# Performance work log

Measured on AMD Instinct MI355X. Metric: run time of the kernel, lower is better.

The kernel has to match this reference:

```python
import jax, jax.numpy as jnp
import numpy as np

D = 768        # word_emb_dim * 3 (span embedding dim)
H = 1024       # assumed FFNNScore hidden width
K = 250        # antecedent window (self.k)
P_LAMBDA = 0.4


def setup_inputs() -> dict:
    key = jax.random.key(0)
    ks = jax.random.split(key, 8)
    N, T = 2000, 1000
    return {
        "vectors": jax.random.normal(ks[0], (N, D), jnp.float32),
        "Wm1": jax.random.normal(ks[1], (D, H), jnp.float32) / np.sqrt(D),
        "bm1": jnp.zeros((H,), jnp.float32),
        "wm2": jax.random.normal(ks[2], (H,), jnp.float32) / np.sqrt(H),
        "bm2": jnp.zeros((1,), jnp.float32),
        "Wp1": jax.random.normal(ks[3], (3 * D, H), jnp.float32) / np.sqrt(3 * D),
        "bp1": jnp.zeros((H,), jnp.float32),
        "wp2": jax.random.normal(ks[4], (H,), jnp.float32) / np.sqrt(H),
        "bp2": jnp.zeros((1,), jnp.float32),
        "span_starts": jax.random.randint(ks[5], (N,), 0, T, dtype=jnp.int32),
        "span_ends": jax.random.randint(ks[6], (N,), 0, T, dtype=jnp.int32),
        "t": T,
    }


def reference(vectors, Wm1, bm1, wm2, bm2, Wp1, bp1, wp2, bp2,
              span_starts, span_ends, t):
    m = int(P_LAMBDA * t)  # number of retained spans (static)

    # mention scorer: FFNN over all span embeddings  [N]
    scores = jax.nn.relu(vectors @ Wm1 + bm1) @ wm2 + bm2[0]

    # prune to top int(p_lambda * t) spans by mention score (descending sort)
    top = jnp.argsort(-scores)[:m]
    s_top, v_top = scores[top], vectors[top]

    # re-sort retained spans by (i_start, i_end) descending
    order = jnp.lexsort((span_ends[top], span_starts[top]))[::-1]
    v, s = v_top[order], s_top[order]  # [m, D], [m]

    # pairwise scorer weight split for cat([a, b, a*b]) @ Wp1
    Wa, Wb, Wab = Wp1[:D], Wp1[D:2 * D], Wp1[2 * D:]

    # antecedent windows: span i vs spans i+1 .. i+K (padded/masked)
    idx = jnp.arange(m - 1)[:, None] + 1 + jnp.arange(K)[None, :]  # [m-1, K]
    valid = idx < m
    idxc = jnp.minimum(idx, m - 1)

    a = v[:m - 1]                      # [m-1, D]
    b = v[idxc]                        # [m-1, K, D]
    hb = (v @ Wb)[idxc]                # gather precomputed b-projection [m-1, K, H]
    h = jax.nn.relu((a @ Wa)[:, None, :] + hb
                    + jnp.einsum('ikd,dh->ikh', a[:, None, :] * b, Wab)
                    + bp1)             # [m-1, K, H]
    pairwise = h @ wp2 + bp2[0]        # [m-1, K]

    ant = pairwise + s[idxc] + s[:m - 1, None]
    ant = jnp.where(valid, ant, -jnp.inf)
    # dummy antecedent (epsilon) score 0 appended, then softmax per span
    full = jnp.concatenate([ant, jnp.zeros((m - 1, 1), ant.dtype)], axis=1)
    return jax.nn.softmax(full, axis=-1)  # [m-1, K+1]
```

## Files before the change

kernel.cpp:

```cpp
#include <hip/hip_runtime.h>
#include <hip/hip_bf16.h>
#include <math.h>

#define NVEC 2000
#define DD   768
#define HH   1024
#define KNUM 250
#define MSEL 400
#define MR   399
#define OUTW 251
#define PPAD 256
#define NPAIR (MR * PPAD)
#define BM 128
#define BN 256
#define BK 64
#define NKT (DD / BK)
#define NNB (HH / BN)
#define KH1 271
#define PAIRBLKS (MR + KH1)

typedef short  bf16x8 __attribute__((ext_vector_type(8)));
typedef float  f32x4  __attribute__((ext_vector_type(4)));
typedef unsigned int u32;
typedef u32    u32x4  __attribute__((ext_vector_type(4)));

__device__ __forceinline__ float waveSum(float p) {
#pragma unroll
  for (int off = 32; off >= 1; off >>= 1) p += __shfl_xor(p, off, 64);
  return p;
}
__device__ __forceinline__ float waveMax(float p) {
#pragma unroll
  for (int off = 32; off >= 1; off >>= 1) p = fmaxf(p, __shfl_xor(p, off, 64));
  return p;
}
__device__ __forceinline__ short f2bf(float f) {
  __hip_bfloat16 h = __float2bfloat16(f);
  return __builtin_bit_cast(short, h);
}
__device__ __forceinline__ void gload_lds16(const void* g, void* l) {
  __builtin_amdgcn_global_load_lds(
      (const __attribute__((address_space(1))) u32*)g,
      (__attribute__((address_space(3))) u32*)l, 16, 0, 0);
}
__device__ __forceinline__ bf16x8 prodcvt(const float* av, bf16x8 b) {
  u32x4 u = __builtin_bit_cast(u32x4, b);
  bf16x8 r;
#pragma unroll
  for (int p = 0; p < 4; ++p) {
    const float blo = __builtin_bit_cast(float, u[p] << 16);
    const float bhi = __builtin_bit_cast(float, u[p] & 0xffff0000u);
    r[2 * p]     = f2bf(av[2 * p]     * blo);
    r[2 * p + 1] = f2bf(av[2 * p + 1] * bhi);
  }
  return r;
}

__global__ __launch_bounds__(512) void scores_kernel(
    const float* __restrict__ vectors, const float* __restrict__ Wm1,
    const float* __restrict__ bm1, const float* __restrict__ wm2,
    const float* __restrict__ bm2, float* __restrict__ scores) {
  __shared__ float vrow[8 * DD];
  __shared__ float red[8];
  const int tid = threadIdx.x;
  const int base = blockIdx.x * 8;
  for (int idx = tid; idx < 8 * DD; idx += 512)
    vrow[idx] = vectors[base * DD + idx];
  __syncthreads();
  float acc[8][2];
#pragma unroll
  for (int r = 0; r < 8; ++r) { acc[r][0] = 0.f; acc[r][1] = 0.f; }
#pragma unroll 4
  for (int d = 0; d < DD; ++d) {
    const float2 w = ((const float2*)(Wm1 + (size_t)d * HH))[tid];
#pragma unroll
    for (int r = 0; r < 8; ++r) {
      const float a = vrow[r * DD + d];
      acc[r][0] += a * w.x; acc[r][1] += a * w.y;
    }
  }
  const float2 b = ((const float2*)bm1)[tid];
  const float2 m = ((const float2*)wm2)[tid];
  const float sc = bm2[0];
  for (int r = 0; r < 8; ++r) {
    float p = fmaxf(acc[r][0] + b.x, 0.f) * m.x + fmaxf(acc[r][1] + b.y, 0.f) * m.y;
    p = waveSum(p);
    if ((tid & 63) == 0) red[tid >> 6] = p;
    __syncthreads();
    if (tid == 0) {
      float t = red[0];
#pragma unroll
      for (int w8 = 1; w8 < 8; ++w8) t += red[w8];
      scores[base + r] = t + sc;
    }
    __syncthreads();
  }
}

__global__ __launch_bounds__(1024) void sortwt_kernel(
    const float* __restrict__ scores, const int* __restrict__ sst,
    const int* __restrict__ sen, const float* __restrict__ Wp1,
    int* __restrict__ perm, float* __restrict__ sfin, ushort* __restrict__ Wt) {
  const int tid = threadIdx.x;
  if (blockIdx.x == 0) {
    __shared__ float ks[2048];
    __shared__ int   ki[2048];
    __shared__ int s_st[512], s_en[512], s_j[512];
    for (int e = tid; e < 2048; e += 1024) {
      ks[e] = (e < NVEC) ? scores[e] : -INFINITY;
      ki[e] = e;
    }
    __syncthreads();
    for (int k = 2; k <= 2048; k <<= 1) {
      for (int j = k >> 1; j > 0; j >>= 1) {
        for (int e = tid; e < 2048; e += 1024) {
          const int l = e ^ j;
          if (l > e) {
            const float s1 = ks[e], s2 = ks[l];
            const int i1 = ki[e], i2 = ki[l];
            const bool first = (s1 > s2) || (s1 == s2 && i1 < i2);
            const bool up = ((e & k) == 0);
            if (up ? !first : first) {
              ks[e] = s2; ks[l] = s1; ki[e] = i2; ki[l] = i1;
            }
          }
        }
        __syncthreads();
      }
    }
    for (int e = tid; e < 512; e += 1024) {
      if (e < MSEL) { const int ti = ki[e]; s_st[e] = sst[ti]; s_en[e] = sen[ti]; }
      else { s_st[e] = 0x7fffffff; s_en[e] = 0x7fffffff; }
      s_j[e] = e;
    }
    __syncthreads();
    for (int k = 2; k <= 512; k <<= 1) {
      for (int j = k >> 1; j > 0; j >>= 1) {
        for (int e = tid; e < 512; e += 1024) {
          const int l = e ^ j;
          if (l > e) {
            const int a0 = s_st[e], a1 = s_en[e], a2 = s_j[e];
            const int b0 = s_st[l], b1 = s_en[l], b2 = s_j[l];
            const bool first = (a0 < b0) || (a0 == b0 && (a1 < b1 || (a1 == b1 && a2 < b2)));
            const bool up = ((e & k) == 0);
            if (up ? !first : first) {
              s_st[e] = b0; s_en[e] = b1; s_j[e] = b2;
              s_st[l] = a0; s_en[l] = a1; s_j[l] = a2;
            }
          }
        }
        __syncthreads();
      }
    }
    for (int i = tid; i < MSEL; i += 1024) {
      const int src = s_j[MSEL - 1 - i];
      const int vi = ki[src];
      perm[i] = vi;
      sfin[i] = scores[vi];
    }
  } else {
    __shared__ float tile[64][65];
    const int t2 = blockIdx.x - 1;
    const int kb = t2 % 12;
    const int nb = t2 / 12;
    const float* Wab = Wp1 + 2 * DD * HH;
    for (int idx = tid; idx < 64 * 64; idx += 1024) {
      const int kk = idx >> 6, nn = idx & 63;
      tile[kk][nn] = Wab[(size_t)(kb * 64 + kk) * HH + nb * 64 + nn];
    }
    __syncthreads();
    for (int idx = tid; idx < 64 * 64; idx += 1024) {
      const int nn = idx >> 6, kk = idx & 63;
      Wt[(size_t)(nb * 64 + nn) * DD + kb * 64 + kk] = (ushort)f2bf(tile[kk][nn]);
    }
  }
}

__global__ __launch_bounds__(512) void hab_kernel(
    const float* __restrict__ vectors, const float* __restrict__ Wp1,
    const int* __restrict__ perm, float* __restrict__ Ha, float* __restrict__ Hv,
    float* __restrict__ Vp, ushort* __restrict__ Vpb) {
  __shared__ float vrow[8 * DD];
  const int tid = threadIdx.x;
  const int base = blockIdx.x * 8;
  const int mat = blockIdx.y >> 1;
  const int half = blockIdx.y & 1;
  for (int r = 0; r < 8; ++r) {
    const int pi = perm[base + r];
    for (int d = tid; d < DD; d += 512) {
      const float val = vectors[pi * DD + d];
      vrow[r * DD + d] = val;
      if (blockIdx.y == 0) {
        Vp[(size_t)(base + r) * DD + d] = val;
        Vpb[(size_t)(base + r) * DD + d] = (ushort)f2bf(val);
      }
    }
  }
  __syncthreads();
  float acc[8];
#pragma unroll
  for (int r = 0; r < 8; ++r) acc[r] = 0.f;
  const float* W = Wp1 + (size_t)mat * DD * HH + half * 512 + tid;
#pragma unroll 4
  for (int d = 0; d < DD; ++d) {
    const float w = W[(size_t)d * HH];
#pragma unroll
    for (int r = 0; r < 8; ++r) acc[r] += vrow[r * DD + d] * w;
  }
  float* dst = mat ? Hv : Ha;
  for (int r = 0; r < 8; ++r) {
    const int row = base + r;
    if (mat == 0 && row >= MR) continue;
    dst[(size_t)row * HH + half * 512 + tid] = acc[r];
  }
}

__global__ __launch_bounds__(512, 2) void pair_kernel(
    const float* __restrict__ Vp, const ushort* __restrict__ Vpb,
    const ushort* __restrict__ Wt,
    const float* __restrict__ bp1, const float* __restrict__ wp2,
    const float* __restrict__ Ha, const float* __restrict__ Hv,
    float* __restrict__ pp) {
  __shared__ __align__(16) ushort As[BM * BK];
  __shared__ __align__(16) ushort Bs[BN * BK];
  __shared__ float redp[BM][4];
  const int tid = threadIdx.x;
  const int bx = blockIdx.x;
  const int khalf = (bx < MR) ? 0 : 1;
  const int i = (bx < MR) ? bx : (bx - MR);
  const int nb = blockIdx.y;
  const int n0 = nb * BN;
  const int lane = tid & 63;
  const int wid = tid >> 6;
  const int wr = wid >> 2, wc = wid & 3;
  const int lhi = lane >> 4, llo = lane & 15;

  const int cs = tid & 7;
  const int rb9 = tid >> 3;
  const int csx = cs ^ (rb9 & 7);
  const ushort* vsrc[2];
  int rowA[2];
#pragma unroll
  for (int it = 0; it < 2; ++it) {
    rowA[it] = it * 64 + rb9;
    int j = i + 1 + khalf * BM + rowA[it];
    if (j > MR) j = MR;
    vsrc[it] = Vpb + (size_t)j * DD + cs * 8;
  }
  int rowB[4];
#pragma unroll
  for (int it = 0; it < 4; ++it) rowB[it] = it * 64 + rb9;
  const float* avp = Vp + (size_t)i * DD + cs * 8;

  f32x4 acc[4][4];
#pragma unroll
  for (int a = 0; a < 4; ++a)
#pragma unroll
    for (int b = 0; b < 4; ++b) acc[a][b] = (f32x4){0.f, 0.f, 0.f, 0.f};

  for (int kt = 0; kt < NKT; ++kt) {
    const int kg = kt * BK;
    bf16x8 bv[2];
    float av[8];
#pragma unroll
    for (int it = 0; it < 2; ++it) bv[it] = *(const bf16x8*)(vsrc[it] + kg);
    *(float4*)(av) = *(const float4*)(avp + kg);
    *(float4*)(av + 4) = *(const float4*)(avp + kg + 4);
#pragma unroll
    for (int it = 0; it < 4; ++it)
      gload_lds16(Wt + (size_t)(n0 + rowB[it]) * DD + kg + csx * 8,
                  (char*)Bs + (it * 512 + tid) * 16);
#pragma unroll
    for (int it = 0; it < 2; ++it)
      *(bf16x8*)((char*)As + rowA[it] * 128 + (csx << 4)) = prodcvt(av, bv[it]);
    __syncthreads();
#pragma unroll
    for (int ks = 0; ks < 2; ++ks) {
      bf16x8 af[4], bfr[4];
#pragma unroll
      for (int mi = 0; mi < 4; ++mi) {
        const int row = wr * 64 + mi * 16 + llo;
        const int ch = (ks * 4 + lhi) ^ (row & 7);
        af[mi] = *(const bf16x8*)((const char*)As + row * 128 + (ch << 4));
      }
#pragma unroll
      for (int ni = 0; ni < 4; ++ni) {
        const int row = wc * 64 + ni * 16 + llo;
        const int ch = (ks * 4 + lhi) ^ (row & 7);
        bfr[ni] = *(const bf16x8*)((const char*)Bs + row * 128 + (ch << 4));
      }
#pragma unroll
      for (int mi = 0; mi < 4; ++mi)
#pragma unroll
        for (int ni = 0; ni < 4; ++ni)
          acc[mi][ni] = __builtin_amdgcn_mfma_f32_16x16x32_bf16(af[mi], bfr[ni], acc[mi][ni], 0, 0, 0);
    }
    __syncthreads();
  }

  float hb4[4], wpv[4];
  int cg[4];
#pragma unroll
  for (int ni = 0; ni < 4; ++ni) {
    const int col = n0 + wc * 64 + ni * 16 + llo;
    cg[ni] = col;
    hb4[ni] = Ha[(size_t)i * HH + col] + bp1[col];
    wpv[ni] = wp2[col];
  }
#pragma unroll
  for (int mi = 0; mi < 4; ++mi) {
#pragma unroll
    for (int r = 0; r < 4; ++r) {
      const int rowl = wr * 64 + mi * 16 + lhi * 4 + r;
      int j = i + 1 + khalf * BM + rowl;
      if (j > MR) j = MR;
      float part = 0.f;
#pragma unroll
      for (int ni = 0; ni < 4; ++ni) {
        const float pre = acc[mi][ni][r] + hb4[ni] + Hv[(size_t)j * HH + cg[ni]];
        part += fmaxf(pre, 0.f) * wpv[ni];
      }
      part += __shfl_xor(part, 1, 64);
      part += __shfl_xor(part, 2, 64);
      part += __shfl_xor(part, 4, 64);
      part += __shfl_xor(part, 8, 64);
      if (llo == 0) redp[rowl][wc] = part;
    }
  }
  __syncthreads();
  if (tid < BM)
    pp[(size_t)nb * NPAIR + (size_t)i * PPAD + khalf * BM + tid] =
        redp[tid][0] + redp[tid][1] + redp[tid][2] + redp[tid][3];
}

__global__ __launch_bounds__(256) void softmax_kernel(
    const float* __restrict__ pp, const float* __restrict__ sfin,
    const float* __restrict__ bp2, float* __restrict__ out) {
  __shared__ float red[4];
  const int i = blockIdx.x, tid = threadIdx.x;
  float v;
  if (tid < KNUM) {
    const int jidx = i + 1 + tid;
    const bool valid = jidx < MSEL;
    const int jc = valid ? jidx : MR;
    float s = 0.f;
#pragma unroll
    for (int b = 0; b < NNB; ++b) s += pp[(size_t)b * NPAIR + i * PPAD + tid];
    v = valid ? (s + bp2[0] + sfin[jc] + sfin[i]) : -INFINITY;
  } else if (tid == KNUM) v = 0.f;
  else v = -INFINITY;
  float mx = waveMax(v);
  if ((tid & 63) == 0) red[tid >> 6] = mx;
  __syncthreads();
  const float m = fmaxf(fmaxf(red[0], red[1]), fmaxf(red[2], red[3]));
  __syncthreads();
  const float e = (tid <= KNUM) ? expf(v - m) : 0.f;
  float s = waveSum(e);
  if ((tid & 63) == 0) red[tid >> 6] = s;
  __syncthreads();
  const float tot = red[0] + red[1] + red[2] + red[3];
  if (tid <= KNUM) out[i * OUTW + tid] = e / tot;
}

extern "C" void kernel_launch(void* const* d_in, const int* in_sizes, int n_in,
                              void* d_out, int out_size, void* d_ws, size_t ws_size,
                              hipStream_t stream) {
  const float* vectors = (const float*)d_in[0];
  const float* Wm1 = (const float*)d_in[1];
  const float* bm1 = (const float*)d_in[2];
  const float* wm2 = (const float*)d_in[3];
  const float* bm2 = (const float*)d_in[4];
  const float* Wp1 = (const float*)d_in[5];
  const float* bp1 = (const float*)d_in[6];
  const float* wp2 = (const float*)d_in[7];
  const float* bp2 = (const float*)d_in[8];
  const int* sst = (const int*)d_in[9];
  const int* sen = (const int*)d_in[10];
  float* out = (float*)d_out;
  char* ws = (char*)d_ws;

  float* scores = (float*)(ws);
  int*   perm   = (int*)(ws + 10240);
  float* sfin   = (float*)(ws + 12288);
  float* Ha     = (float*)(ws + 16384);
  float* Hv     = (float*)(ws + 16384 + 1638400);
  float* Vp     = (float*)(ws + 3293184);
  ushort* Wt    = (ushort*)(ws + 4521984);
  ushort* Vpb   = (ushort*)(ws + 6094848);
  float* pp     = (float*)(ws + 6709248);

  scores_kernel<<<NVEC / 8, 512, 0, stream>>>(vectors, Wm1, bm1, wm2, bm2, scores);
  sortwt_kernel<<<193, 1024, 0, stream>>>(scores, sst, sen, Wp1, perm, sfin, Wt);
  hab_kernel<<<dim3(MSEL / 8, 4), 512, 0, stream>>>(vectors, Wp1, perm, Ha, Hv, Vp, Vpb);
  pair_kernel<<<dim3(PAIRBLKS, NNB), 512, 0, stream>>>(Vp, Vpb, Wt, bp1, wp2, Ha, Hv, pp);
  softmax_kernel<<<MR, 256, 0, stream>>>(pp, sfin, bp2, out);
}
```

Before: 357.0 us.

## Fuse softmax into pair kernel via last-block atomic counter; split scores over H

The softmax kernel is removed. Each pair block increments a per-row atomic counter after writing its partial, and the last block to arrive for a row does the reduction and softmax. This saves one launch and its tail. The scores kernel now splits the hidden dimension across two blocks with 16 rows each. The two partial sums are combined, with the bias added, in the sort kernel. This reshapes the scores grid and data reuse, at the cost of atomics, fences and an extra done-buffer reset in hab_kernel.

```diff
diff --git a/kernel.cpp b/kernel.cpp
--- a/kernel.cpp
+++ b/kernel.cpp
@@ -59,31 +59,29 @@
 __global__ __launch_bounds__(512) void scores_kernel(
     const float* __restrict__ vectors, const float* __restrict__ Wm1,
     const float* __restrict__ bm1, const float* __restrict__ wm2,
-    const float* __restrict__ bm2, float* __restrict__ scores) {
-  __shared__ float vrow[8 * DD];
+    float* __restrict__ spart) {
+  __shared__ float vrow[16 * DD];
   __shared__ float red[8];
   const int tid = threadIdx.x;
-  const int base = blockIdx.x * 8;
-  for (int idx = tid; idx < 8 * DD; idx += 512)
+  const int base = blockIdx.x * 16;
+  const int half = blockIdx.y;
+  for (int idx = tid; idx < 16 * DD; idx += 512)
     vrow[idx] = vectors[base * DD + idx];
   __syncthreads();
-  float acc[8][2];
-#pragma unroll
-  for (int r = 0; r < 8; ++r) { acc[r][0] = 0.f; acc[r][1] = 0.f; }
+  float acc[16];
+#pragma unroll
+  for (int r = 0; r < 16; ++r) acc[r] = 0.f;
+  const float* W = Wm1 + half * 512 + tid;
 #pragma unroll 4
   for (int d = 0; d < DD; ++d) {
-    const float2 w = ((const float2*)(Wm1 + (size_t)d * HH))[tid];
-#pragma unroll
-    for (int r = 0; r < 8; ++r) {
-      const float a = vrow[r * DD + d];
-      acc[r][0] += a * w.x; acc[r][1] += a * w.y;
-    }
-  }
-  const float2 b = ((const float2*)bm1)[tid];
-  const float2 m = ((const float2*)wm2)[tid];
-  const float sc = bm2[0];
-  for (int r = 0; r < 8; ++r) {
-    float p = fmaxf(acc[r][0] + b.x, 0.f) * m.x + fmaxf(acc[r][1] + b.y, 0.f) * m.y;
+    const float w = W[(size_t)d * HH];
+#pragma unroll
+    for (int r = 0; r < 16; ++r) acc[r] += vrow[r * DD + d] * w;
+  }
+  const float b = bm1[half * 512 + tid];
+  const float m = wm2[half * 512 + tid];
+  for (int r = 0; r < 16; ++r) {
+    float p = fmaxf(acc[r] + b, 0.f) * m;
     p = waveSum(p);
     if ((tid & 63) == 0) red[tid >> 6] = p;
     __syncthreads();
@@ -91,23 +89,26 @@
       float t = red[0];
 #pragma unroll
       for (int w8 = 1; w8 < 8; ++w8) t += red[w8];
-      scores[base + r] = t + sc;
+      spart[(size_t)(base + r) * 2 + half] = t;
     }
     __syncthreads();
   }
 }
 
 __global__ __launch_bounds__(1024) void sortwt_kernel(
-    const float* __restrict__ scores, const int* __restrict__ sst,
-    const int* __restrict__ sen, const float* __restrict__ Wp1,
+    const float* __restrict__ spart, const int* __restrict__ sst,
+    const int* __restrict__ sen, const float* __restrict__ bm2,
+    const float* __restrict__ Wp1,
     int* __restrict__ perm, float* __restrict__ sfin, ushort* __restrict__ Wt) {
   const int tid = threadIdx.x;
   if (blockIdx.x == 0) {
     __shared__ float ks[2048];
     __shared__ int   ki[2048];
     __shared__ int s_st[512], s_en[512], s_j[512];
+    const float bm2v = bm2[0];
     for (int e = tid; e < 2048; e += 1024) {
-      ks[e] = (e < NVEC) ? scores[e] : -INFINITY;
+      ks[e] = (e < NVEC) ? (spart[(size_t)e * 2] + spart[(size_t)e * 2 + 1] + bm2v)
+                         : -INFINITY;
       ki[e] = e;
     }
     __syncthreads();
@@ -156,7 +157,7 @@
       const int src = s_j[MSEL - 1 - i];
       const int vi = ki[src];
       perm[i] = vi;
-      sfin[i] = scores[vi];
+      sfin[i] = spart[(size_t)vi * 2] + spart[(size_t)vi * 2 + 1] + bm2v;
     }
   } else {
     __shared__ float tile[64][65];
@@ -179,12 +180,13 @@
 __global__ __launch_bounds__(512) void hab_kernel(
     const float* __restrict__ vectors, const float* __restrict__ Wp1,
     const int* __restrict__ perm, float* __restrict__ Ha, float* __restrict__ Hv,
-    float* __restrict__ Vp, ushort* __restrict__ Vpb) {
+    float* __restrict__ Vp, ushort* __restrict__ Vpb, int* __restrict__ done) {
   __shared__ float vrow[8 * DD];
   const int tid = threadIdx.x;
   const int base = blockIdx.x * 8;
   const int mat = blockIdx.y >> 1;
   const int half = blockIdx.y & 1;
+  if (blockIdx.x == 0 && blockIdx.y == 0 && tid < MR) done[tid] = 0;
   for (int r = 0; r < 8; ++r) {
     const int pi = perm[base + r];
     for (int d = tid; d < DD; d += 512) {
@@ -220,10 +222,13 @@
     const ushort* __restrict__ Wt,
     const float* __restrict__ bp1, const float* __restrict__ wp2,
     const float* __restrict__ Ha, const float* __restrict__ Hv,
-    float* __restrict__ pp) {
+    const float* __restrict__ sfin, const float* __restrict__ bp2,
+    float* __restrict__ pp, int* __restrict__ done, float* __restrict__ out) {
   __shared__ __align__(16) ushort As[BM * BK];
   __shared__ __align__(16) ushort Bs[BN * BK];
   __shared__ float redp[BM][4];
+  __shared__ float sred[8];
+  __shared__ int sdone;
   const int tid = threadIdx.x;
   const int bx = blockIdx.x;
   const int khalf = (bx < MR) ? 0 : 1;
@@ -331,35 +336,43 @@
   if (tid < BM)
     pp[(size_t)nb * NPAIR + (size_t)i * PPAD + khalf * BM + tid] =
         redp[tid][0] + redp[tid][1] + redp[tid][2] + redp[tid][3];
-}
-
-__global__ __launch_bounds__(256) void softmax_kernel(
-    const float* __restrict__ pp, const float* __restrict__ sfin,
-    const float* __restrict__ bp2, float* __restrict__ out) {
-  __shared__ float red[4];
-  const int i = blockIdx.x, tid = threadIdx.x;
-  float v;
-  if (tid < KNUM) {
-    const int jidx = i + 1 + tid;
-    const bool valid = jidx < MSEL;
-    const int jc = valid ? jidx : MR;
-    float s = 0.f;
-#pragma unroll
-    for (int b = 0; b < NNB; ++b) s += pp[(size_t)b * NPAIR + i * PPAD + tid];
-    v = valid ? (s + bp2[0] + sfin[jc] + sfin[i]) : -INFINITY;
-  } else if (tid == KNUM) v = 0.f;
-  else v = -INFINITY;
-  float mx = waveMax(v);
-  if ((tid & 63) == 0) red[tid >> 6] = mx;
+
   __syncthreads();
-  const float m = fmaxf(fmaxf(red[0], red[1]), fmaxf(red[2], red[3]));
+  if (tid == 0) {
+    __threadfence();
+    sdone = atomicAdd(&done[i], 1);
+  }
   __syncthreads();
-  const float e = (tid <= KNUM) ? expf(v - m) : 0.f;
-  float s = waveSum(e);
-  if ((tid & 63) == 0) red[tid >> 6] = s;
-  __syncthreads();
-  const float tot = red[0] + red[1] + red[2] + red[3];
-  if (tid <= KNUM) out[i * OUTW + tid] = e / tot;
+  const int tgt = (i < KH1) ? 8 : 4;
+  if (sdone == tgt - 1) {
+    __threadfence();
+    float v;
+    if (tid < KNUM) {
+      const int jidx = i + 1 + tid;
+      const bool valid = jidx < MSEL;
+      const int jc = valid ? jidx : MR;
+      float s = 0.f;
+#pragma unroll
+      for (int b = 0; b < NNB; ++b) s += pp[(size_t)b * NPAIR + (size_t)i * PPAD + tid];
+      v = valid ? (s + bp2[0] + sfin[jc] + sfin[i]) : -INFINITY;
+    } else if (tid == KNUM) v = 0.f;
+    else v = -INFINITY;
+    float mx = waveMax(v);
+    if ((tid & 63) == 0) sred[tid >> 6] = mx;
+    __syncthreads();
+    float m = sred[0];
+#pragma unroll
+    for (int w8 = 1; w8 < 8; ++w8) m = fmaxf(m, sred[w8]);
+    __syncthreads();
+    const float e = (tid <= KNUM) ? expf(v - m) : 0.f;
+    float s2 = waveSum(e);
+    if ((tid & 63) == 0) sred[tid >> 6] = s2;
+    __syncthreads();
+    float tot = sred[0];
+#pragma unroll
+    for (int w8 = 1; w8 < 8; ++w8) tot += sred[w8];
+    if (tid <= KNUM) out[(size_t)i * OUTW + tid] = e / tot;
+  }
 }
 
 extern "C" void kernel_launch(void* const* d_in, const int* in_sizes, int n_in,
@@ -379,19 +392,20 @@
   float* out = (float*)d_out;
   char* ws = (char*)d_ws;
 
-  float* scores = (float*)(ws);
-  int*   perm   = (int*)(ws + 10240);
-  float* sfin   = (float*)(ws + 12288);
-  float* Ha     = (float*)(ws + 16384);
-  float* Hv     = (float*)(ws + 16384 + 1638400);
-  float* Vp     = (float*)(ws + 3293184);
-  ushort* Wt    = (ushort*)(ws + 4521984);
-  ushort* Vpb   = (ushort*)(ws + 6094848);
-  float* pp     = (float*)(ws + 6709248);
-
-  scores_kernel<<<NVEC / 8, 512, 0, stream>>>(vectors, Wm1, bm1, wm2, bm2, scores);
-  sortwt_kernel<<<193, 1024, 0, stream>>>(scores, sst, sen, Wp1, perm, sfin, Wt);
-  hab_kernel<<<dim3(MSEL / 8, 4), 512, 0, stream>>>(vectors, Wp1, perm, Ha, Hv, Vp, Vpb);
-  pair_kernel<<<dim3(PAIRBLKS, NNB), 512, 0, stream>>>(Vp, Vpb, Wt, bp1, wp2, Ha, Hv, pp);
-  softmax_kernel<<<MR, 256, 0, stream>>>(pp, sfin, bp2, out);
-}
+  float* spart = (float*)(ws);
+  int*   perm  = (int*)(ws + 16384);
+  float* sfin  = (float*)(ws + 18432);
+  float* Ha    = (float*)(ws + 20480);
+  float* Hv    = (float*)(ws + 1658880);
+  float* Vp    = (float*)(ws + 3297280);
+  ushort* Wt   = (ushort*)(ws + 4526080);
+  ushort* Vpb  = (ushort*)(ws + 6098944);
+  float* pp    = (float*)(ws + 6713344);
+  int*   done  = (int*)(ws + 8347648);
+
+  scores_kernel<<<dim3(125, 2), 512, 0, stream>>>(vectors, Wm1, bm1, wm2, spart);
+  sortwt_kernel<<<193, 1024, 0, stream>>>(spart, sst, sen, bm2, Wp1, perm, sfin, Wt);
+  hab_kernel<<<dim3(MSEL / 8, 4), 512, 0, stream>>>(vectors, Wp1, perm, Ha, Hv, Vp, Vpb, done);
+  pair_kernel<<<dim3(PAIRBLKS, NNB), 512, 0, stream>>>(
+      Vp, Vpb, Wt, bp1, wp2, Ha, Hv, sfin, bp2, pp, done, out);
+}
```

Measured after the change: 449.4 us. 25.9% more time.
